# Kernel tuning notes

Measured on AMD Instinct MI355X. Metric: run time of the kernel, lower is better.

Reference implementation:

```python
import jax, jax.numpy as jnp
import numpy as np

N, E, D, L = 100000, 1_600_000, 128, 8


def setup_inputs() -> dict:
    key = jax.random.key(0)
    k0, k1, k2 = jax.random.split(key, 3)
    x = jax.random.normal(k0, (N, D), dtype=jnp.float32)
    edge_index = jax.random.randint(k1, (2, E), 0, N, dtype=jnp.int64)
    Ws = jax.random.normal(k2, (L, D, D), dtype=jnp.float32) / np.float32(np.sqrt(D))
    bs = jnp.zeros((L, D), dtype=jnp.float32)
    return {"x": x, "edge_index": edge_index, "Ws": Ws, "bs": bs}


def _gcn_conv(h, W, b, src, dst, norm_edge, self_norm):
    """PyG GCNConv: linear -> sym-normalized aggregate (with self loops) -> +bias."""
    h = h @ W                                    # [N, D]
    msg = h[src] * norm_edge[:, None]            # [E, D] gather + scale
    agg = jax.ops.segment_sum(msg, dst, num_segments=h.shape[0])  # scatter-add
    return agg + h * self_norm[:, None] + b      # self-loop term fused in


def reference(x, edge_index, Ws, bs):
    src, dst = edge_index[0], edge_index[1]
    # degree of (A + I) on target nodes, symmetric normalization
    deg = jax.ops.segment_sum(jnp.ones((src.shape[0],), jnp.float32), dst,
                              num_segments=x.shape[0]) + 1.0
    dis = deg ** -0.5                            # deg >= 1, safe
    norm_edge = dis[src] * dis[dst]              # per-edge norm
    self_norm = dis * dis                        # per-node self-loop norm

    n_layers = Ws.shape[0]
    h = x
    initial = x
    for i in range(n_layers):
        h = _gcn_conv(h, Ws[i], bs[i], src, dst, norm_edge, self_norm)
        if i > 0:
            h = h + initial
            initial = h
        h = jax.nn.relu(h)
        if i < n_layers - 1:
            # NOTE: at i == 0 the original indexes layers[-1] (last layer) — faithful.
            j = i - 1
            h = h + _gcn_conv(h, Ws[j], bs[j], src, dst, norm_edge, self_norm)
    return h
```

## Files before the change

### kernel.cpp

```cpp
#include <hip/hip_runtime.h>

#define D 128
#define SCAN_CH 1024
#define SA_STRIDE 136
#define SC_STRIDE 132
#define NPB 64
#define CONV_THREADS 512

typedef _Float16 f16x8 __attribute__((ext_vector_type(8)));
typedef float f32x4 __attribute__((ext_vector_type(4)));


__global__ void hist_kernel(const int* __restrict__ dst, int* __restrict__ counts,
                            int E, int N) {
  int range = blockIdx.x & 7;
  int lo = (int)(((long long)N * range) >> 3);
  int hi = (int)(((long long)N * (range + 1)) >> 3);
  int stride = (gridDim.x >> 3) * blockDim.x;
  for (int e = (blockIdx.x >> 3) * blockDim.x + threadIdx.x; e < E; e += stride) {
    int d = dst[e];
    if (d >= lo && d < hi) atomicAdd(&counts[d], 1);
  }
}

__global__ void fill_kernel(const int* __restrict__ src, const int* __restrict__ dst,
    int* __restrict__ fillp, int* __restrict__ csr_src, int E, int N) {
  int range = blockIdx.x & 7;
  int lo = (int)(((long long)N * range) >> 3);
  int hi = (int)(((long long)N * (range + 1)) >> 3);
  int stride = (gridDim.x >> 3) * blockDim.x;
  for (int e = (blockIdx.x >> 3) * blockDim.x + threadIdx.x; e < E; e += stride) {
    int d = dst[e];
    if (d >= lo && d < hi) {
      int s = src[e];
      int p = atomicAdd(&fillp[d], 1);
      csr_src[p] = s;
    }
  }
}

__global__ void dis_kernel(const int* __restrict__ counts, float2* __restrict__ dnr, int N) {
  int n = blockIdx.x * blockDim.x + threadIdx.x;
  if (n < N) {
    float c = (float)counts[n] + 1.0f;
    dnr[n] = make_float2(rsqrtf(c), sqrtf(c));
  }
}

__global__ __launch_bounds__(256) void scan_phaseA(const int* __restrict__ counts,
    int* __restrict__ blksum, int N) {
  __shared__ int red[256];
  int base = blockIdx.x * SCAN_CH;
  int t = threadIdx.x;
  int s = 0;
  #pragma unroll
  for (int j = 0; j < 4; ++j) {
    int idx = base + t * 4 + j;
    if (idx < N) s += counts[idx];
  }
  red[t] = s;
  __syncthreads();
  for (int d = 128; d > 0; d >>= 1) {
    if (t < d) red[t] += red[t + d];
    __syncthreads();
  }
  if (t == 0) blksum[blockIdx.x] = red[0];
}

__global__ __launch_bounds__(1024) void scan_phaseB(int* __restrict__ blksum, int NB) {
  __shared__ int sa[1024], sb[1024];
  int t = threadIdx.x;
  int v = (t < NB) ? blksum[t] : 0;
  sa[t] = v;
  __syncthreads();
  int* a = sa; int* b = sb;
  for (int d = 1; d < 1024; d <<= 1) {
    int val = a[t] + ((t >= d) ? a[t - d] : 0);
    b[t] = val;
    __syncthreads();
    int* tmp = a; a = b; b = tmp;
  }
  if (t < NB) blksum[t] = a[t] - v;
}

__global__ __launch_bounds__(256) void scan_phaseC(const int* __restrict__ counts,
    const int* __restrict__ blksum, int* __restrict__ row_ptr, int* __restrict__ fillp, int N) {
  __shared__ int ra[256], rb[256];
  int base = blockIdx.x * SCAN_CH;
  int t = threadIdx.x;
  int v[4]; int s = 0;
  #pragma unroll
  for (int j = 0; j < 4; ++j) {
    int idx = base + t * 4 + j;
    v[j] = (idx < N) ? counts[idx] : 0;
    s += v[j];
  }
  ra[t] = s;
  __syncthreads();
  int* a = ra; int* b = rb;
  for (int d = 1; d < 256; d <<= 1) {
    int val = a[t] + ((t >= d) ? a[t - d] : 0);
    b[t] = val;
    __syncthreads();
    int* tmp = a; a = b; b = tmp;
  }
  int excl = a[t] - s + blksum[blockIdx.x];
  #pragma unroll
  for (int j = 0; j < 4; ++j) {
    int idx = base + t * 4 + j;
    if (idx < N) {
      row_ptr[idx] = excl;
      fillp[idx] = excl;
      excl += v[j];
      if (idx == N - 1) row_ptr[N] = excl;
    }
  }
}


__global__ void conv_x_kernel(const float* __restrict__ x, const float2* __restrict__ dnr,
    _Float16* __restrict__ hs, _Float16* __restrict__ x16, int total8) {
  int i = blockIdx.x * blockDim.x + threadIdx.x;
  if (i >= total8) return;
  int node = i >> 4;
  float dn = dnr[node].x;
  const float4* p = (const float4*)(x + (size_t)i * 8);
  float4 a = p[0], b = p[1];
  f16x8 v, w;
  v[0] = (_Float16)(dn * a.x); v[1] = (_Float16)(dn * a.y);
  v[2] = (_Float16)(dn * a.z); v[3] = (_Float16)(dn * a.w);
  v[4] = (_Float16)(dn * b.x); v[5] = (_Float16)(dn * b.y);
  v[6] = (_Float16)(dn * b.z); v[7] = (_Float16)(dn * b.w);
  w[0] = (_Float16)a.x; w[1] = (_Float16)a.y; w[2] = (_Float16)a.z; w[3] = (_Float16)a.w;
  w[4] = (_Float16)b.x; w[5] = (_Float16)b.y; w[6] = (_Float16)b.z; w[7] = (_Float16)b.w;
  *(f16x8*)(hs + (size_t)i * 8) = v;
  *(f16x8*)(x16 + (size_t)i * 8) = w;
}

__global__ void repack_w_kernel(const float* __restrict__ Ws, _Float16* __restrict__ Wf, int total) {
  int t = blockIdx.x * blockDim.x + threadIdx.x;
  if (t >= total) return;
  int lane = t & 63;
  int nb = (t >> 6) & 7;
  int kb = (t >> 9) & 3;
  int l = t >> 11;
  int col = nb * 16 + (lane & 15);
  int k0 = kb * 32 + (lane >> 4) * 8;
  const float* w = Ws + (size_t)l * D * D;
  f16x8 v;
  #pragma unroll
  for (int j = 0; j < 8; ++j) v[j] = (_Float16)w[(k0 + j) * D + col];
  *(f16x8*)(Wf + (size_t)t * 8) = v;
}

__global__ __launch_bounds__(CONV_THREADS) void conv_fused_kernel(
    const _Float16* __restrict__ hs, const int* __restrict__ row_ptr,
    const int* __restrict__ csr_src, const float2* __restrict__ dnr,
    const f16x8* __restrict__ Wf, const float* __restrict__ bias,
    const _Float16* __restrict__ init16in, _Float16* __restrict__ init16out,
    float* __restrict__ out, _Float16* __restrict__ hs_out, int N, int flags) {
  __shared__ __align__(16) char smem[NPB * SC_STRIDE * 4];
  _Float16* sA = (_Float16*)smem;
  float* sC = (float*)smem;
  int tid = threadIdx.x;
  int node0 = blockIdx.x * NPB;
  int ng = tid >> 4;
  int li = tid & 15;
  int c0 = li * 8;
  int wave = tid >> 6, lane = tid & 63;

  f16x8 bf[4];
  #pragma unroll
  for (int kb = 0; kb < 4; ++kb)
    bf[kb] = Wf[(kb * 8 + wave) * 64 + lane];

  float2 dr[2];
  f16x8 ownr[2];

  #pragma unroll
  for (int k = 0; k < 2; ++k) {
    int lr = ng + 32 * k;
    int n = node0 + lr;
    f16x8 g = {};
    if (n < N) {
      float acc[8];
      #pragma unroll
      for (int j = 0; j < 8; ++j) acc[j] = 0.f;
      int beg = row_ptr[n], end = row_ptr[n + 1];
      #pragma unroll 8
      for (int e = beg; e < end; ++e) {
        int s = csr_src[e];
        f16x8 v = *(const f16x8*)&hs[(size_t)s * D + c0];
        #pragma unroll
        for (int j = 0; j < 8; ++j) acc[j] += (float)v[j];
      }
      f16x8 own = *(const f16x8*)&hs[(size_t)n * D + c0];
      float2 d2 = dnr[n];
      dr[k] = d2;
      ownr[k] = own;
      #pragma unroll
      for (int j = 0; j < 8; ++j) g[j] = (_Float16)(d2.x * (acc[j] + (float)own[j]));
    }
    *(f16x8*)&sA[lr * SA_STRIDE + c0] = g;
  }
  __syncthreads();

  f32x4 ca[4];
  #pragma unroll
  for (int rt = 0; rt < 4; ++rt) ca[rt] = (f32x4){0, 0, 0, 0};
  #pragma unroll
  for (int rt = 0; rt < 4; ++rt) {
    #pragma unroll
    for (int kb = 0; kb < 4; ++kb) {
      f16x8 a = *(const f16x8*)&sA[(rt * 16 + (lane & 15)) * SA_STRIDE + kb * 32 + (lane >> 4) * 8];
      ca[rt] = __builtin_amdgcn_mfma_f32_16x16x32_f16(a, bf[kb], ca[rt], 0, 0, 0);
    }
  }
  __syncthreads();

  {
    int colb = wave * 16 + (lane & 15);
    int rowb = (lane >> 4) * 4;
    #pragma unroll
    for (int rt = 0; rt < 4; ++rt)
      #pragma unroll
      for (int r = 0; r < 4; ++r)
        sC[(rt * 16 + rowb + r) * SC_STRIDE + colb] = ca[rt][r];
  }
  __syncthreads();

  float4 b0 = *(const float4*)&bias[c0];
  float4 b1 = *(const float4*)&bias[c0 + 4];
  #pragma unroll
  for (int k = 0; k < 2; ++k) {
    int lr = ng + 32 * k;
    int n = node0 + lr;
    if (n >= N) continue;
    float v[8];
    float4 s0 = *(const float4*)&sC[lr * SC_STRIDE + c0];
    float4 s1 = *(const float4*)&sC[lr * SC_STRIDE + c0 + 4];
    v[0] = s0.x + b0.x; v[1] = s0.y + b0.y; v[2] = s0.z + b0.z; v[3] = s0.w + b0.w;
    v[4] = s1.x + b1.x; v[5] = s1.y + b1.y; v[6] = s1.z + b1.z; v[7] = s1.w + b1.w;
    size_t off = (size_t)n * D + c0;
    if (flags & 8) {
      float rd = dr[k].y;
      #pragma unroll
      for (int j = 0; j < 8; ++j) v[j] += (float)ownr[k][j] * rd;
    }
    if (flags & 1) {
      f16x8 iv = *(const f16x8*)&init16in[off];
      #pragma unroll
      for (int j = 0; j < 8; ++j) v[j] += (float)iv[j];
    }
    if (flags & 2) {
      f16x8 o;
      #pragma unroll
      for (int j = 0; j < 8; ++j) o[j] = (_Float16)v[j];
      *(f16x8*)&init16out[off] = o;
    }
    if (flags & 4) {
      #pragma unroll
      for (int j = 0; j < 8; ++j) v[j] = fmaxf(v[j], 0.f);
    }
    if (flags & 32) {
      *(float4*)&out[off]     = make_float4(v[0], v[1], v[2], v[3]);
      *(float4*)&out[off + 4] = make_float4(v[4], v[5], v[6], v[7]);
    }
    if (flags & 16) {
      float dn = dr[k].x;
      f16x8 h8;
      #pragma unroll
      for (int j = 0; j < 8; ++j) h8[j] = (_Float16)(dn * v[j]);
      *(f16x8*)&hs_out[off] = h8;
    }
  }
}


extern "C" void kernel_launch(void* const* d_in, const int* in_sizes, int n_in,
                              void* d_out, int out_size, void* d_ws, size_t ws_size,
                              hipStream_t stream) {
  const float* x = (const float*)d_in[0];
  const int* ei = (const int*)d_in[1];
  const float* Ws = (const float*)d_in[2];
  const float* bs = (const float*)d_in[3];
  float* out = (float*)d_out;

  const int N = in_sizes[0] / D;
  const int E = in_sizes[1] / 2;
  const int L = in_sizes[2] / (D * D);
  const int* src = ei;
  const int* dst = ei + E;

  uintptr_t p = (uintptr_t)d_ws;
  auto alloc = [&](size_t bytes) {
    uintptr_t r = p;
    p = (r + bytes + 255) & ~(uintptr_t)255;
    return r;
  };
  float2*    dnr      = (float2*)alloc((size_t)N * 8);
  int*       counts   = (int*)  alloc((size_t)N * 4);
  int*       row_ptr  = (int*)  alloc((size_t)(N + 1) * 4);
  int*       fillp    = (int*)  alloc((size_t)N * 4);
  int*       blksum   = (int*)  alloc((size_t)1024 * 4);
  int*       csr_src  = (int*)  alloc((size_t)E * 4);
  _Float16*  hs_a     = (_Float16*)alloc((size_t)N * D * 2);
  _Float16*  hs_b     = (_Float16*)alloc((size_t)N * D * 2);
  _Float16*  init16   = (_Float16*)alloc((size_t)N * D * 2);
  _Float16*  Wf       = (_Float16*)alloc((size_t)L * 4 * 8 * 64 * 8 * 2);

  const int NB = (N + SCAN_CH - 1) / SCAN_CH;

  hipMemsetAsync(counts, 0, (size_t)N * 4, stream);
  hist_kernel<<<8 * 192, 256, 0, stream>>>(dst, counts, E, N);
  dis_kernel<<<(N + 255) / 256, 256, 0, stream>>>(counts, dnr, N);
  scan_phaseA<<<NB, 256, 0, stream>>>(counts, blksum, N);
  scan_phaseB<<<1, 1024, 0, stream>>>(blksum, NB);
  scan_phaseC<<<NB, 256, 0, stream>>>(counts, blksum, row_ptr, fillp, N);
  fill_kernel<<<8 * 192, 256, 0, stream>>>(src, dst, fillp, csr_src, E, N);
  conv_x_kernel<<<(N * 16 + 255) / 256, 256, 0, stream>>>(x, dnr, hs_a, init16, N * 16);
  {
    int total = L * 2048;
    repack_w_kernel<<<(total + 255) / 256, 256, 0, stream>>>(Ws, Wf, total);
  }

  const int conv_grid = (N + NPB - 1) / NPB;
  _Float16* hsp[2] = {hs_a, hs_b};
  int cur = 0;

  for (int i = 0; i < L; ++i) {
    int flags;
    if (i == 0)          flags = 4 | 16;
    else if (i == L - 1) flags = 1 | 4 | 32;
    else                 flags = 1 | 2 | 4 | 16;
    conv_fused_kernel<<<conv_grid, CONV_THREADS, 0, stream>>>(hsp[cur], row_ptr, csr_src,
        dnr, (const f16x8*)(Wf + (size_t)i * 2048 * 8), bs + (size_t)i * D,
        init16, init16, out, hsp[cur ^ 1], N, flags);
    if (flags & 16) cur ^= 1;
    if (i < L - 1) {
      int j = (i == 0) ? (L - 1) : (i - 1);
      conv_fused_kernel<<<conv_grid, CONV_THREADS, 0, stream>>>(hsp[cur], row_ptr, csr_src,
          dnr, (const f16x8*)(Wf + (size_t)j * 2048 * 8), bs + (size_t)j * D,
          init16, init16, out, hsp[cur ^ 1], N, 8 | 16);
      cur ^= 1;
    }
  }
}
```

Before: 1.367 ms.

## Split each node's edge gather across four lane groups with shuffle reduction

The CSR aggregation now assigns each wave eight nodes and splits each node's edge list across four 16-lane groups. Each group accumulates a strided subset of edges, two at a time, and the partial sums are combined with cross-lane xor shuffles. The goal is more memory-level parallelism and less serial latency per node, and better load balance than one 16-thread group walking a whole neighbor list. In exchange the own-row and norm values are reloaded in the epilogue instead of kept in registers, and 3/4 of the lanes idle during the final write.

```diff
diff --git a/kernel.cpp b/kernel.cpp
--- a/kernel.cpp
+++ b/kernel.cpp
@@ -164,44 +164,53 @@
   float* sC = (float*)smem;
   int tid = threadIdx.x;
   int node0 = blockIdx.x * NPB;
-  int ng = tid >> 4;
-  int li = tid & 15;
+  int wave = tid >> 6, lane = tid & 63;
+  int es = lane >> 4;
+  int li = lane & 15;
   int c0 = li * 8;
-  int wave = tid >> 6, lane = tid & 63;
 
   f16x8 bf[4];
   #pragma unroll
   for (int kb = 0; kb < 4; ++kb)
     bf[kb] = Wf[(kb * 8 + wave) * 64 + lane];
 
-  float2 dr[2];
-  f16x8 ownr[2];
-
-  #pragma unroll
-  for (int k = 0; k < 2; ++k) {
-    int lr = ng + 32 * k;
+  #pragma unroll 2
+  for (int k = 0; k < 8; ++k) {
+    int lr = wave * 8 + k;
     int n = node0 + lr;
-    f16x8 g = {};
-    if (n < N) {
-      float acc[8];
-      #pragma unroll
-      for (int j = 0; j < 8; ++j) acc[j] = 0.f;
-      int beg = row_ptr[n], end = row_ptr[n + 1];
-      #pragma unroll 8
-      for (int e = beg; e < end; ++e) {
-        int s = csr_src[e];
-        f16x8 v = *(const f16x8*)&hs[(size_t)s * D + c0];
-        #pragma unroll
-        for (int j = 0; j < 8; ++j) acc[j] += (float)v[j];
-      }
+    if (n >= N) break;
+    float acc[8];
+    #pragma unroll
+    for (int j = 0; j < 8; ++j) acc[j] = 0.f;
+    int beg = row_ptr[n], end = row_ptr[n + 1];
+    int e = beg + es;
+    for (; e + 4 < end; e += 8) {
+      int s0 = csr_src[e];
+      int s1 = csr_src[e + 4];
+      f16x8 v0 = *(const f16x8*)&hs[(size_t)s0 * D + c0];
+      f16x8 v1 = *(const f16x8*)&hs[(size_t)s1 * D + c0];
+      #pragma unroll
+      for (int j = 0; j < 8; ++j) acc[j] += (float)v0[j] + (float)v1[j];
+    }
+    for (; e < end; e += 4) {
+      int s = csr_src[e];
+      f16x8 v = *(const f16x8*)&hs[(size_t)s * D + c0];
+      #pragma unroll
+      for (int j = 0; j < 8; ++j) acc[j] += (float)v[j];
+    }
+    #pragma unroll
+    for (int j = 0; j < 8; ++j) {
+      acc[j] += __shfl_xor(acc[j], 16, 64);
+      acc[j] += __shfl_xor(acc[j], 32, 64);
+    }
+    if (es == 0) {
       f16x8 own = *(const f16x8*)&hs[(size_t)n * D + c0];
-      float2 d2 = dnr[n];
-      dr[k] = d2;
-      ownr[k] = own;
-      #pragma unroll
-      for (int j = 0; j < 8; ++j) g[j] = (_Float16)(d2.x * (acc[j] + (float)own[j]));
-    }
-    *(f16x8*)&sA[lr * SA_STRIDE + c0] = g;
+      float dn = dnr[n].x;
+      f16x8 g;
+      #pragma unroll
+      for (int j = 0; j < 8; ++j) g[j] = (_Float16)(dn * (acc[j] + (float)own[j]));
+      *(f16x8*)&sA[lr * SA_STRIDE + c0] = g;
+    }
   }
   __syncthreads();
 
@@ -229,6 +238,7 @@
   }
   __syncthreads();
 
+  int ng = tid >> 4;
   float4 b0 = *(const float4*)&bias[c0];
   float4 b1 = *(const float4*)&bias[c0 + 4];
   #pragma unroll
@@ -242,10 +252,12 @@
     v[0] = s0.x + b0.x; v[1] = s0.y + b0.y; v[2] = s0.z + b0.z; v[3] = s0.w + b0.w;
     v[4] = s1.x + b1.x; v[5] = s1.y + b1.y; v[6] = s1.z + b1.z; v[7] = s1.w + b1.w;
     size_t off = (size_t)n * D + c0;
+    float2 d2 = dnr[n];
     if (flags & 8) {
-      float rd = dr[k].y;
-      #pragma unroll
-      for (int j = 0; j < 8; ++j) v[j] += (float)ownr[k][j] * rd;
+      f16x8 own = *(const f16x8*)&hs[off];
+      float rd = d2.y;
+      #pragma unroll
+      for (int j = 0; j < 8; ++j) v[j] += (float)own[j] * rd;
     }
     if (flags & 1) {
       f16x8 iv = *(const f16x8*)&init16in[off];
@@ -267,7 +279,7 @@
       *(float4*)&out[off + 4] = make_float4(v[4], v[5], v[6], v[7]);
     }
     if (flags & 16) {
-      float dn = dr[k].x;
+      float dn = d2.x;
       f16x8 h8;
       #pragma unroll
       for (int j = 0; j < 8; ++j) h8[j] = (_Float16)(dn * v[j]);
```

New measurement: 1.582 ms. 1.16x slower.
